# Kernel optimization log

Measured on AMD Instinct MI355X. Metric: run time of the kernel, lower is better.

Reference implementation:

```python
import jax, jax.numpy as jnp
import numpy as np

NUM_CLASSES = 1000
FEAT_DIM = 256
N = 262144
ALPHA = 0.5


def setup_inputs() -> dict:
    key = jax.random.key(0)
    k1, k2, k3 = jax.random.split(key, 3)
    features = jax.random.normal(k1, (N, FEAT_DIM), dtype=jnp.float32)
    labels = jax.random.randint(k2, (N,), 0, NUM_CLASSES, dtype=jnp.int64)
    centers = jax.random.normal(k3, (NUM_CLASSES, FEAT_DIM), dtype=jnp.float32)
    return {"features": features, "labels": labels, "centers": centers}


def reference(features, labels, centers):
    # Fused segment-mean: scatter-add of features + per-class counts,
    # replacing the per-class python loop in the original.
    sums = jax.ops.segment_sum(features, labels, num_segments=NUM_CLASSES)  # [C, D]
    counts = jax.ops.segment_sum(
        jnp.ones((features.shape[0],), dtype=features.dtype),
        labels,
        num_segments=NUM_CLASSES,
    )  # [C]
    has_samples = counts > 0
    safe_counts = jnp.where(has_samples, counts, 1.0)
    class_means = sums / safe_counts[:, None]  # [C, D]
    # EMA update only for classes present in the batch.
    updated = (1.0 - ALPHA) * centers + ALPHA * class_means
    new_centers = jnp.where(has_samples[:, None], updated, centers)
    return new_centers
```

## Files before the change

### kernel.cpp

```cpp
#include <hip/hip_runtime.h>

constexpr int N   = 262144;
constexpr int C   = 1000;
constexpr int CP  = 1024;
constexpr int D   = 256;
constexpr int D4  = 64;
constexpr int NG  = 32;
constexpr int NSL = 16;
constexpr int NBLK = NG * NSL;
constexpr int ROWS_PER_SLICE = N / NSL;
constexpr int CLS_PER_BLK  = CP / NG;
constexpr int CLS_PER_WAVE = CLS_PER_BLK / 8;
constexpr int SCAN_PER_WAVE = ROWS_PER_SLICE / 8;
constexpr int CAP = 96;
constexpr float ALPHA = 0.5f;

typedef float vfloat4 __attribute__((ext_vector_type(4)));


__global__ __launch_bounds__(512, 4) void accum_kernel(
        const vfloat4* __restrict__ feat4,
        const int*     __restrict__ labels,
        float*         __restrict__ partials,
        int*           __restrict__ counts_p) {
    __shared__ int lists[CLS_PER_BLK][CAP];
    __shared__ int cursor[CLS_PER_BLK];

    const int bid  = blockIdx.x;
    const int g    = bid >> 4;
    const int s    = bid & 15;
    const int tid  = threadIdx.x;
    const int w    = tid >> 6;
    const int lane = tid & 63;

    if (tid < CLS_PER_BLK) cursor[tid] = 0;
    __syncthreads();

    const int wbase = s * ROWS_PER_SLICE + w * SCAN_PER_WAVE;
    for (int i = 0; i < SCAN_PER_WAVE; i += 64) {
        const int row = wbase + i + lane;
        const int lab = labels[row];
        if ((lab >> 5) == g) {
            const int cl  = lab & 31;
            const int pos = atomicAdd(&cursor[cl], 1);
            if (pos < CAP) lists[cl][pos] = row;
        }
    }
    __syncthreads();

    #pragma unroll
    for (int cc = 0; cc < CLS_PER_WAVE; ++cc) {
        const int cl  = w * CLS_PER_WAVE + cc;
        const int cnt = cursor[cl];
        const int m   = cnt < CAP ? cnt : CAP;
        vfloat4 acc = (vfloat4)0.f;
        int j = 0;
        for (; j + 4 <= m; j += 4) {
            const int r0 = lists[cl][j + 0];
            const int r1 = lists[cl][j + 1];
            const int r2 = lists[cl][j + 2];
            const int r3 = lists[cl][j + 3];
            vfloat4 v0 = __builtin_nontemporal_load(&feat4[(size_t)r0 * D4 + lane]);
            vfloat4 v1 = __builtin_nontemporal_load(&feat4[(size_t)r1 * D4 + lane]);
            vfloat4 v2 = __builtin_nontemporal_load(&feat4[(size_t)r2 * D4 + lane]);
            vfloat4 v3 = __builtin_nontemporal_load(&feat4[(size_t)r3 * D4 + lane]);
            acc += v0; acc += v1; acc += v2; acc += v3;
        }
        for (; j < m; ++j) {
            const int r = lists[cl][j];
            acc += __builtin_nontemporal_load(&feat4[(size_t)r * D4 + lane]);
        }
        const int gc = g * CLS_PER_BLK + cl;
        vfloat4* outp = (vfloat4*)partials + ((size_t)s * CP + gc) * D4;
        outp[lane] = acc;
        if (lane == 0) counts_p[s * CP + gc] = cnt;
    }
}

__global__ __launch_bounds__(256) void finalize_kernel(
        const float* __restrict__ partials,
        const int*   __restrict__ counts_p,
        const vfloat4* __restrict__ cen4,
        vfloat4*       __restrict__ out4) {
    const int c    = blockIdx.x * 4 + (threadIdx.x >> 6);
    const int lane = threadIdx.x & 63;

    vfloat4 ssum = (vfloat4)0.f;
    #pragma unroll
    for (int sl = 0; sl < NSL; ++sl)
        ssum += ((const vfloat4*)partials)[((size_t)sl * CP + c) * D4 + lane];
    int cnt = 0;
    #pragma unroll
    for (int sl = 0; sl < NSL; ++sl)
        cnt += counts_p[sl * CP + c];

    const vfloat4 cen = cen4[c * D4 + lane];
    vfloat4 o = cen;
    if (cnt > 0) o = (1.0f - ALPHA) * cen + ssum * (ALPHA / (float)cnt);
    out4[c * D4 + lane] = o;
}

extern "C" void kernel_launch(void* const* d_in, const int* in_sizes, int n_in,
                              void* d_out, int out_size, void* d_ws, size_t ws_size,
                              hipStream_t stream) {
    const vfloat4* feat4   = (const vfloat4*)d_in[0];
    const int*     labels  = (const int*)d_in[1];
    const vfloat4* cen4    = (const vfloat4*)d_in[2];
    vfloat4*       out4    = (vfloat4*)d_out;

    float* partials = (float*)d_ws;
    int*   counts_p = (int*)(partials + (size_t)NSL * CP * D);

    accum_kernel<<<NBLK, 512, 0, stream>>>(feat4, labels, partials, counts_p);
    finalize_kernel<<<C / 4, 256, 0, stream>>>(partials, counts_p, cen4, out4);
}
```

Measured before the change: 364.6 us.

## Vectorize label scan and interleave four class gathers per wave

The label scan now reads int4 vectors across the whole block instead of scalar labels per wave, so it issues fewer memory instructions. The gather phase processes a wave's four classes together, two rows each per iteration, with masked weights, putting eight independent row loads in flight instead of four. Invalid slots load row 0 with a zero weight, which adds some redundant traffic and raises register pressure.

```diff
diff --git a/kernel.cpp b/kernel.cpp
--- a/kernel.cpp
+++ b/kernel.cpp
@@ -11,7 +11,6 @@
 constexpr int ROWS_PER_SLICE = N / NSL;
 constexpr int CLS_PER_BLK  = CP / NG;
 constexpr int CLS_PER_WAVE = CLS_PER_BLK / 8;
-constexpr int SCAN_PER_WAVE = ROWS_PER_SLICE / 8;
 constexpr int CAP = 96;
 constexpr float ALPHA = 0.5f;
 
@@ -36,44 +35,66 @@
     if (tid < CLS_PER_BLK) cursor[tid] = 0;
     __syncthreads();
 
-    const int wbase = s * ROWS_PER_SLICE + w * SCAN_PER_WAVE;
-    for (int i = 0; i < SCAN_PER_WAVE; i += 64) {
-        const int row = wbase + i + lane;
-        const int lab = labels[row];
-        if ((lab >> 5) == g) {
-            const int cl  = lab & 31;
-            const int pos = atomicAdd(&cursor[cl], 1);
-            if (pos < CAP) lists[cl][pos] = row;
-        }
+    const int sbase = s * ROWS_PER_SLICE;
+    const int4* lab4 = (const int4*)(labels + sbase);
+    for (int i = tid; i < ROWS_PER_SLICE / 4; i += 512) {
+        const int4 L  = lab4[i];
+        const int  rb = sbase + i * 4;
+        if ((L.x >> 5) == g) { int p = atomicAdd(&cursor[L.x & 31], 1); if (p < CAP) lists[L.x & 31][p] = rb + 0; }
+        if ((L.y >> 5) == g) { int p = atomicAdd(&cursor[L.y & 31], 1); if (p < CAP) lists[L.y & 31][p] = rb + 1; }
+        if ((L.z >> 5) == g) { int p = atomicAdd(&cursor[L.z & 31], 1); if (p < CAP) lists[L.z & 31][p] = rb + 2; }
+        if ((L.w >> 5) == g) { int p = atomicAdd(&cursor[L.w & 31], 1); if (p < CAP) lists[L.w & 31][p] = rb + 3; }
     }
     __syncthreads();
 
+    const int k0 = w * CLS_PER_WAVE;
+    int cnt_[4], m_[4];
     #pragma unroll
-    for (int cc = 0; cc < CLS_PER_WAVE; ++cc) {
-        const int cl  = w * CLS_PER_WAVE + cc;
-        const int cnt = cursor[cl];
-        const int m   = cnt < CAP ? cnt : CAP;
-        vfloat4 acc = (vfloat4)0.f;
-        int j = 0;
-        for (; j + 4 <= m; j += 4) {
-            const int r0 = lists[cl][j + 0];
-            const int r1 = lists[cl][j + 1];
-            const int r2 = lists[cl][j + 2];
-            const int r3 = lists[cl][j + 3];
-            vfloat4 v0 = __builtin_nontemporal_load(&feat4[(size_t)r0 * D4 + lane]);
-            vfloat4 v1 = __builtin_nontemporal_load(&feat4[(size_t)r1 * D4 + lane]);
-            vfloat4 v2 = __builtin_nontemporal_load(&feat4[(size_t)r2 * D4 + lane]);
-            vfloat4 v3 = __builtin_nontemporal_load(&feat4[(size_t)r3 * D4 + lane]);
-            acc += v0; acc += v1; acc += v2; acc += v3;
+    for (int k = 0; k < 4; ++k) {
+        cnt_[k] = cursor[k0 + k];
+        m_[k]   = cnt_[k] < CAP ? cnt_[k] : CAP;
+    }
+    int jmax = m_[0];
+    #pragma unroll
+    for (int k = 1; k < 4; ++k) jmax = m_[k] > jmax ? m_[k] : jmax;
+
+    vfloat4 a0 = (vfloat4)0.f, a1 = (vfloat4)0.f,
+            a2 = (vfloat4)0.f, a3 = (vfloat4)0.f;
+
+    for (int j = 0; j < jmax; j += 2) {
+        int   r[4][2];
+        float wt[4][2];
+        #pragma unroll
+        for (int k = 0; k < 4; ++k)
+            #pragma unroll
+            for (int u = 0; u < 2; ++u) {
+                const bool val = (j + u) < m_[k];
+                r[k][u]  = val ? lists[k0 + k][j + u] : 0;
+                wt[k][u] = val ? 1.f : 0.f;
+            }
+        vfloat4 v[4][2];
+        #pragma unroll
+        for (int k = 0; k < 4; ++k)
+            #pragma unroll
+            for (int u = 0; u < 2; ++u)
+                v[k][u] = __builtin_nontemporal_load(
+                              &feat4[(size_t)r[k][u] * D4 + lane]);
+        #pragma unroll
+        for (int u = 0; u < 2; ++u) {
+            a0 += v[0][u] * wt[0][u];
+            a1 += v[1][u] * wt[1][u];
+            a2 += v[2][u] * wt[2][u];
+            a3 += v[3][u] * wt[3][u];
         }
-        for (; j < m; ++j) {
-            const int r = lists[cl][j];
-            acc += __builtin_nontemporal_load(&feat4[(size_t)r * D4 + lane]);
-        }
-        const int gc = g * CLS_PER_BLK + cl;
+    }
+
+    const vfloat4 accs[4] = {a0, a1, a2, a3};
+    #pragma unroll
+    for (int k = 0; k < 4; ++k) {
+        const int gc = g * CLS_PER_BLK + k0 + k;
         vfloat4* outp = (vfloat4*)partials + ((size_t)s * CP + gc) * D4;
-        outp[lane] = acc;
-        if (lane == 0) counts_p[s * CP + gc] = cnt;
+        outp[lane] = accs[k];
+        if (lane == 0) counts_p[s * CP + gc] = cnt_[k];
     }
 }
 
```

Result: faster. 352.5 us (-3.3%).
